# Kernel tuning notes

Hardware: AMD Instinct MI355X
Metric: run time of the kernel (lower is better)

## Reference

```python
import jax, jax.numpy as jnp
import numpy as np

H, HKV, D, W = 64, 8, 64, 128          # heads, kv heads, head_dim, sliding window
G = H // HKV                            # query heads per kv head
HID = 2880
THETA = 150000.0
SCALE = D ** -0.5
NEG = -1e30


def _rope(x, positions):
    # x: [B,S,h,D]; GPT-NeoX style rotate_half RoPE
    half = D // 2
    inv_freq = 1.0 / (THETA ** (jnp.arange(0, half, dtype=jnp.float32) / half))
    ang = positions.astype(jnp.float32)[:, None] * inv_freq          # [S, D/2]
    cos = jnp.cos(ang)[None, :, None, :]
    sin = jnp.sin(ang)[None, :, None, :]
    x1, x2 = x[..., :half], x[..., half:]
    return jnp.concatenate([x1 * cos - x2 * sin, x2 * cos + x1 * sin], axis=-1)


def setup_inputs() -> dict:
    key = jax.random.key(0)
    ks = jax.random.split(key, 6)
    B, S = 1, 2048
    return {
        "hidden_states": jax.random.normal(ks[0], (B, S, HID), jnp.float32),
        "positions": jnp.arange(S, dtype=jnp.int32),
        "w_qkv": jax.random.normal(ks[1], (HID, (H + 2 * HKV) * D), jnp.float32) * 0.02,
        "b_qkv": jax.random.normal(ks[2], ((H + 2 * HKV) * D,), jnp.float32) * 0.02,
        "w_o": jax.random.normal(ks[3], (H * D, HID), jnp.float32) * 0.02,
        "b_o": jax.random.normal(ks[4], (HID,), jnp.float32) * 0.02,
        "sinks": jax.random.normal(ks[5], (H,), jnp.float32),
    }


def reference(hidden_states, positions, w_qkv, b_qkv, w_o, b_o, sinks):
    B, S, _ = hidden_states.shape
    qkv = hidden_states @ w_qkv + b_qkv                               # [B,S,(H+2Hkv)*D]
    q, k, v = jnp.split(qkv, [H * D, H * D + HKV * D], axis=-1)
    Q = q.reshape(B, S, H, D)
    K = k.reshape(B, S, HKV, D)
    V = v.reshape(B, S, HKV, D)
    Q = _rope(Q, positions)
    K = _rope(K, positions)

    # banded (sliding-window) key/value gather: query i sees keys i-W+1..i
    offsets = jnp.arange(W) - (W - 1)                                 # [-(W-1)..0]
    kidx = jnp.arange(S)[:, None] + offsets                           # [S,W]
    valid = kidx >= 0
    kidx = jnp.maximum(kidx, 0)
    Kw = K[:, kidx]                                                    # [B,S,W,HKV,D]
    Vw = V[:, kidx]

    Qr = Q.reshape(B, S, HKV, G, D)                                    # GQA grouping
    scores = jnp.einsum('bskgd,bswkd->bskgw', Qr, Kw) * SCALE          # [B,S,HKV,G,W]
    scores = jnp.where(valid[None, :, None, None, :], scores, NEG)

    sink = sinks.reshape(HKV, G)[None, None]                           # [1,1,HKV,G]
    m = jnp.maximum(scores.max(axis=-1), sink)                         # [B,S,HKV,G]
    p = jnp.exp(scores - m[..., None])
    denom = p.sum(axis=-1) + jnp.exp(sink - m)                         # sink in normalizer
    out = jnp.einsum('bskgw,bswkd->bskgd', p, Vw) / denom[..., None]

    out = out.reshape(B, S, H * D)
    return out @ w_o + b_o
```

## Files before the change

### kernel.cpp

```cpp
#include <hip/hip_runtime.h>

typedef unsigned short u16;
typedef __bf16 bf16x8 __attribute__((ext_vector_type(8)));
typedef float f32x4 __attribute__((ext_vector_type(4)));
typedef unsigned short u16x8 __attribute__((ext_vector_type(8)));

#define QKV_N 5120
#define SEQ 2048
#define ATTN_K 4096
#define KPAD 2944
#define SCALE 0.125f
#define NEGINF -1e30f

__device__ __forceinline__ u16 f2bf(float f) {
  unsigned int u = __builtin_bit_cast(unsigned int, f);
  u = (u + 0x7FFFu + ((u >> 16) & 1u)) >> 16;
  return (u16)u;
}
__device__ __forceinline__ float bf2f(u16 u) {
  unsigned int x = ((unsigned int)u) << 16;
  return __builtin_bit_cast(float, x);
}

#define MFMA16(a, b, c) __builtin_amdgcn_mfma_f32_16x16x32_bf16((a), (b), (c), 0, 0, 0)

__device__ __forceinline__ void gl_lds16(const u16* g, u16* l) {
  __builtin_amdgcn_global_load_lds(
      (const __attribute__((address_space(1))) unsigned int*)(const void*)g,
      (__attribute__((address_space(3))) unsigned int*)(void*)l, 16, 0, 0);
}

__device__ __forceinline__ bf16x8 fragrd(const u16* base, int row, int rb) {
  return *(const bf16x8*)((const char*)(base + row * 32) + rb);
}

__device__ __forceinline__ bf16x8 lds_frag(const u16* mat, int row, int kh, int lg) {
  int off = row * 128 + ((kh * 64 + lg * 16) ^ ((row & 7) << 4));
  return *(const bf16x8*)((const char*)mat + off);
}

__global__ __launch_bounds__(256) void k_rope_table(const int* __restrict__ pos,
                                                    float2* __restrict__ tab) {
  int t = blockIdx.x * 256 + threadIdx.x;
  int s = t >> 5, i = t & 31;
  float freq = powf(150000.0f, -(float)i * (1.0f / 32.0f));
  float ang = (float)pos[s] * freq;
  float sv, cv;
  sincosf(ang, &sv, &cv);
  tab[t] = make_float2(cv, sv);
}

__global__ __launch_bounds__(256) void k_convert_pad(const float* __restrict__ in,
                                                     u16* __restrict__ out) {
  int i = blockIdx.x * 256 + threadIdx.x;
  int r = i / 736, c4 = i - r * 736;
  if (r >= 2048) return;
  ushort4 o = {0, 0, 0, 0};
  if (c4 < 720) {
    float4 v = *(const float4*)(in + (size_t)r * 2880 + c4 * 4);
    o.x = f2bf(v.x); o.y = f2bf(v.y); o.z = f2bf(v.z); o.w = f2bf(v.w);
  }
  ((ushort4*)out)[(size_t)r * 736 + c4] = o;
}

__global__ __launch_bounds__(256) void k_transpose(const float* __restrict__ in,
                                                   u16* __restrict__ out,
                                                   int Kin, int Kout, int Nd, int Npad) {
  __shared__ float tile[32][33];
  int n0 = blockIdx.x * 32, k0 = blockIdx.y * 32;
  int c = threadIdx.x & 31, r0 = threadIdx.x >> 5;
#pragma unroll
  for (int j = 0; j < 4; j++) {
    int r = r0 + j * 8;
    float v = 0.f;
    if (n0 + c < Nd && k0 + r < Kin) v = in[(size_t)(k0 + r) * Nd + n0 + c];
    tile[r][c] = v;
  }
  __syncthreads();
#pragma unroll
  for (int j = 0; j < 4; j++) {
    int rr = r0 + j * 8;
    int n = n0 + rr;
    if (n < Npad) out[(size_t)n * Kout + k0 + c] = f2bf(tile[c][rr]);
  }
}

__global__ __launch_bounds__(256, 2) void k_gemm1(const u16* __restrict__ Ag,
                                                  const u16* __restrict__ Bg,
                                                  const float* __restrict__ bias,
                                                  u16* __restrict__ C) {
  __shared__ u16 lds_[2][18432];
  u16* L = &lds_[0][0];
  const int tid = threadIdx.x;
  const int lane = tid & 63, wave = tid >> 6;
  const int wm = wave >> 1, wn = wave & 1;
  const int lr = lane & 15, lg = lane >> 4;
  const int bid = blockIdx.x;
  const int sb = (bid & 7) * 64 + (bid >> 3);
  const int m0 = (sb >> 5) * 128, n0 = (sb & 31) * 160;

  f32x4 acc[4][5] = {};
  bf16x8 Bf[5], Af0, Af1;

  const int rb = (lg * 16) ^ (((lr >> 1) & 3) << 4);
  const int arow = tid >> 2;
  const int axs = ((tid & 3) ^ ((tid >> 3) & 3)) << 3;

  size_t boff[5];
#pragma unroll
  for (int r_ = 0; r_ < 5; r_++) {
    int e = r_ * 2048 + tid * 8;
    int bkh = (e >= 5120) ? 1 : 0;
    int re = e - bkh * 5120;
    int brow = re >> 5;
    int bch = (re >> 3) & 3;
    int bps = bch ^ ((brow >> 1) & 3);
    boff[r_] = (size_t)(n0 + brow) * KPAD + bkh * 32 + bps * 8;
  }

#define STA(b, kh, kt, r_)                                                      \
  gl_lds16(Ag + (size_t)(m0 + (r_) * 64 + arow) * KPAD + (kt) + (kh) * 32 + axs, \
           L + (b) * 18432 + (kh) * 4096 + (r_) * 2048 + wave * 512)
#define STB(b, kt, r_)                                                          \
  gl_lds16(Bg + boff[r_] + (kt), L + (b) * 18432 + 8192 + (r_) * 2048 + wave * 512)
#define RDB(b, kh)                                                              \
  { _Pragma("unroll") for (int nf = 0; nf < 5; nf++)                            \
      Bf[nf] = fragrd(L + (b) * 18432 + 8192 + (kh) * 5120,                     \
                      wn * 80 + nf * 16 + lr, rb); }
#define RDA(b, kh, mf0_)                                                        \
  { Af0 = fragrd(L + (b) * 18432 + (kh) * 4096, wm * 64 + (mf0_) * 16 + lr, rb); \
    Af1 = fragrd(L + (b) * 18432 + (kh) * 4096, wm * 64 + ((mf0_) + 1) * 16 + lr, rb); }
#define MM(ma, mb)                                                              \
  { __builtin_amdgcn_s_setprio(1);                                              \
    _Pragma("unroll") for (int nf = 0; nf < 5; nf++) {                          \
      acc[ma][nf] = MFMA16(Af0, Bf[nf], acc[ma][nf]);                           \
      acc[mb][nf] = MFMA16(Af1, Bf[nf], acc[mb][nf]); }                         \
    __builtin_amdgcn_s_setprio(0); }
#define BAR __builtin_amdgcn_s_barrier();
#define VM4 asm volatile("s_waitcnt vmcnt(4)" ::: "memory");
#define VM0 asm volatile("s_waitcnt vmcnt(0)" ::: "memory");

  STA(0, 0, 0, 0); STA(0, 0, 0, 1);
  STB(0, 0, 0); STB(0, 0, 1); STB(0, 0, 2); STB(0, 0, 3); STB(0, 0, 4);
  STA(0, 1, 0, 0); STA(0, 1, 0, 1);
  VM4 BAR

  for (int t = 0; t < 46; t++) {
    const int b = t & 1, nb = b ^ 1;
    const int kt1 = (t + 1) * 64;
    const bool st = (t < 45);
    RDB(b, 0) RDA(b, 0, 0)
    if (st) { STA(nb, 0, kt1, 0); STA(nb, 0, kt1, 1); STB(nb, kt1, 0); }
    BAR MM(0, 1) BAR
    RDA(b, 0, 2)
    if (st) { STB(nb, kt1, 1); STB(nb, kt1, 2); VM4 } else { VM0 }
    BAR MM(2, 3) BAR
    RDB(b, 1) RDA(b, 1, 0)
    if (st) { STB(nb, kt1, 3); STB(nb, kt1, 4); }
    BAR MM(0, 1) BAR
    RDA(b, 1, 2)
    if (st) { STA(nb, 1, kt1, 0); STA(nb, 1, kt1, 1); VM4 }
    BAR MM(2, 3) BAR
  }
#undef STA
#undef STB
#undef RDB
#undef RDA
#undef MM
#undef BAR
#undef VM4
#undef VM0

#pragma unroll
  for (int mf = 0; mf < 4; mf++)
#pragma unroll
    for (int nf = 0; nf < 5; nf++) {
      int col = n0 + wn * 80 + nf * 16 + lr;
      float bv = bias[col];
#pragma unroll
      for (int rg = 0; rg < 4; rg++) {
        int row = m0 + wm * 64 + mf * 16 + lg * 4 + rg;
        C[(size_t)row * QKV_N + col] = f2bf(acc[mf][nf][rg] + bv);
      }
    }
}

__global__ __launch_bounds__(256, 2) void k_gemm2(const u16* __restrict__ Ag,
                                                  const u16* __restrict__ Bg,
                                                  const float* __restrict__ bias,
                                                  float* __restrict__ C) {
  __shared__ u16 ldsbuf[2][16384];
  const int tid = threadIdx.x;
  const int lane = tid & 63, wave = tid >> 6;
  const int wm = wave >> 1, wn = wave & 1;
  const int lr = lane & 15, lg = lane >> 4;
  int bid = blockIdx.x;
  int sb = (bid & 7) * 46 + (bid >> 3);
  const int m0 = (sb / 23) * 128, n0 = (sb % 23) * 128;

  f32x4 acc[4][4] = {};

  const int srow = wave * 8 + (lane >> 3);
  const int sc = ((lane & 7) ^ (lane >> 3)) << 3;
  const u16* gA = Ag + (size_t)(m0 + srow) * ATTN_K + sc;
  const u16* gB = Bg + (size_t)(n0 + srow) * ATTN_K + sc;

#define G2_STAGE(kt, b)                                                          \
  {                                                                              \
    u16* Ab = &ldsbuf[b][0];                                                     \
    u16* Bb = &ldsbuf[b][8192];                                                  \
    _Pragma("unroll") for (int r = 0; r < 4; r++) {                              \
      gl_lds16(gA + (size_t)(r * 32) * ATTN_K + (kt), Ab + (r * 32 + wave * 8) * 64); \
      gl_lds16(gB + (size_t)(r * 32) * ATTN_K + (kt), Bb + (r * 32 + wave * 8) * 64); \
    }                                                                            \
  }

  G2_STAGE(0, 0)
  G2_STAGE(64, 1)
  asm volatile("s_waitcnt vmcnt(8)" ::: "memory");
  __builtin_amdgcn_s_barrier();

  for (int t = 0; t < 64; t++) {
    const int b = t & 1;
    const u16* La = &ldsbuf[b][0];
    const u16* Lb = &ldsbuf[b][8192];
    bf16x8 Bf[4][2];
#pragma unroll
    for (int nf = 0; nf < 4; nf++)
#pragma unroll
      for (int kh = 0; kh < 2; kh++)
        Bf[nf][kh] = lds_frag(Lb, wn * 64 + nf * 16 + lr, kh, lg);
    bf16x8 Af[2][2];
#pragma unroll
    for (int mi = 0; mi < 2; mi++)
#pragma unroll
      for (int kh = 0; kh < 2; kh++)
        Af[mi][kh] = lds_frag(La, wm * 64 + mi * 16 + lr, kh, lg);
#pragma unroll
    for (int q = 0; q < 2; q++) {
      bf16x8 An[2][2];
      if (q < 1) {
#pragma unroll
        for (int mi = 0; mi < 2; mi++)
#pragma unroll
          for (int kh = 0; kh < 2; kh++)
            An[mi][kh] = lds_frag(La, wm * 64 + ((q + 1) * 2 + mi) * 16 + lr, kh, lg);
      }
      __builtin_amdgcn_s_setprio(1);
#pragma unroll
      for (int mi = 0; mi < 2; mi++)
#pragma unroll
        for (int nf = 0; nf < 4; nf++)
#pragma unroll
          for (int kh = 0; kh < 2; kh++)
            acc[q * 2 + mi][nf] = MFMA16(Af[mi][kh], Bf[nf][kh], acc[q * 2 + mi][nf]);
      __builtin_amdgcn_s_setprio(0);
      if (q < 1) {
#pragma unroll
        for (int mi = 0; mi < 2; mi++)
#pragma unroll
          for (int kh = 0; kh < 2; kh++)
            Af[mi][kh] = An[mi][kh];
      }
    }
    __builtin_amdgcn_s_barrier();
    if (t <= 61) {
      G2_STAGE((t + 2) * 64, b)
      asm volatile("s_waitcnt vmcnt(8)" ::: "memory");
    } else {
      asm volatile("s_waitcnt vmcnt(0)" ::: "memory");
    }
    __builtin_amdgcn_s_barrier();
  }
#undef G2_STAGE

#pragma unroll
  for (int mi = 0; mi < 4; mi++)
#pragma unroll
    for (int ni = 0; ni < 4; ni++) {
      int row = m0 + wm * 64 + mi * 16 + lg * 4;
      int col = n0 + wn * 64 + ni * 16 + lr;
      if (col < 2880) {
        float bv = bias[col];
#pragma unroll
        for (int rg = 0; rg < 4; rg++)
          C[(size_t)(row + rg) * 2880 + col] = acc[mi][ni][rg] + bv;
      }
    }
}

__global__ __launch_bounds__(512, 2) void k_attn(const u16* __restrict__ qkv,
                                                 const float* __restrict__ sinks,
                                                 const float2* __restrict__ tab,
                                                 u16* __restrict__ out) {
  __shared__ u16 Klds[160 * 64];
  __shared__ u16 Vt[64 * 168];
  __shared__ u16 Pslab[8 * 32 * 40];
  const int hk = blockIdx.y;
  const int s0 = blockIdx.x * 32;
  const int kb = s0 - 127;
  const int tid = threadIdx.x;
  const int lane = tid & 63, w = tid >> 6;
  const int lr = lane & 15, lg = lane >> 4;

  for (int u = tid; u < 160 * 4; u += 512) {
    int key = u >> 2, c = u & 3;
    int kidx = kb + key;
    u16x8 v1 = {0, 0, 0, 0, 0, 0, 0, 0}, v2 = v1;
    if (kidx >= 0 && kidx < SEQ) {
      const u16* base = qkv + (size_t)kidx * QKV_N + 4096 + hk * 64;
      u16x8 x1 = *(const u16x8*)(base + c * 8);
      u16x8 x2 = *(const u16x8*)(base + 32 + c * 8);
      const float2* cs = tab + (size_t)kidx * 32 + c * 8;
#pragma unroll
      for (int j = 0; j < 8; j++) {
        float f1 = bf2f(x1[j]), f2 = bf2f(x2[j]);
        float2 t = cs[j];
        v1[j] = f2bf(f1 * t.x - f2 * t.y);
        v2[j] = f2bf(f2 * t.x + f1 * t.y);
      }
    }
    int o1 = (key * 128 + c * 16) ^ ((key & 7) << 4);
    int o2 = (key * 128 + (c + 4) * 16) ^ ((key & 7) << 4);
    *(u16x8*)((char*)Klds + o1) = v1;
    *(u16x8*)((char*)Klds + o2) = v2;
  }
  for (int e4 = tid; e4 < 160 * 16; e4 += 512) {
    int key = e4 >> 4, d0 = (e4 & 15) * 4;
    int kidx = kb + key;
    ushort4 v = {0, 0, 0, 0};
    if (kidx >= 0 && kidx < SEQ)
      v = *(const ushort4*)(qkv + (size_t)kidx * QKV_N + 4608 + hk * 64 + d0);
    Vt[(d0 + 0) * 168 + key] = v.x;
    Vt[(d0 + 1) * 168 + key] = v.y;
    Vt[(d0 + 2) * 168 + key] = v.z;
    Vt[(d0 + 3) * 168 + key] = v.w;
  }

  const int head = hk * 8 + w;
  bf16x8 qf[2][2];
#pragma unroll
  for (int rt = 0; rt < 2; rt++) {
    int s = s0 + rt * 16 + lr;
    const u16* base = qkv + (size_t)s * QKV_N + head * 64 + lg * 8;
    u16x8 r0 = *(const u16x8*)(base);
    u16x8 r1 = *(const u16x8*)(base + 32);
    const float2* cs = tab + (size_t)s * 32 + lg * 8;
    u16x8 y0, y1;
#pragma unroll
    for (int j = 0; j < 8; j++) {
      float f1 = bf2f(r0[j]), f2 = bf2f(r1[j]);
      float2 t = cs[j];
      y0[j] = f2bf(f1 * t.x - f2 * t.y);
      y1[j] = f2bf(f2 * t.x + f1 * t.y);
    }
    qf[rt][0] = __builtin_bit_cast(bf16x8, y0);
    qf[rt][1] = __builtin_bit_cast(bf16x8, y1);
  }
  __syncthreads();

  f32x4 sc[2][10];
  f32x4 zz = {0.f, 0.f, 0.f, 0.f};
#pragma unroll
  for (int rt = 0; rt < 2; rt++)
#pragma unroll
    for (int nt = 0; nt < 10; nt++) sc[rt][nt] = zz;
#pragma unroll
  for (int nt = 0; nt < 10; nt++) {
    int key = nt * 16 + lr;
#pragma unroll
    for (int ks = 0; ks < 2; ks++) {
      int off = (key * 128 + ks * 64 + lg * 16) ^ ((key & 7) << 4);
      bf16x8 kf = *(const bf16x8*)((const char*)Klds + off);
      sc[0][nt] = MFMA16(qf[0][ks], kf, sc[0][nt]);
      sc[1][nt] = MFMA16(qf[1][ks], kf, sc[1][nt]);
    }
  }

#pragma unroll
  for (int rt = 0; rt < 2; rt++)
#pragma unroll
    for (int nt = 0; nt < 10; nt++)
#pragma unroll
      for (int rg = 0; rg < 4; rg++) {
        int qq = rt * 16 + lg * 4 + rg;
        int j = nt * 16 + lr;
        bool valid = (j >= qq) && (j <= qq + 127) && ((kb + j) >= 0);
        sc[rt][nt][rg] = valid ? sc[rt][nt][rg] * SCALE : NEGINF;
      }

  const float sink = sinks[head];
  float den[2][4];
#pragma unroll
  for (int rt = 0; rt < 2; rt++)
#pragma unroll
    for (int rg = 0; rg < 4; rg++) {
      float m = NEGINF;
#pragma unroll
      for (int nt = 0; nt < 10; nt++) m = fmaxf(m, sc[rt][nt][rg]);
#pragma unroll
      for (int x = 1; x < 16; x <<= 1) m = fmaxf(m, __shfl_xor(m, x, 64));
      m = fmaxf(m, sink);
      float sum = 0.f;
#pragma unroll
      for (int nt = 0; nt < 10; nt++) {
        float p = __expf(sc[rt][nt][rg] - m);
        sc[rt][nt][rg] = p;
        sum += p;
      }
#pragma unroll
      for (int x = 1; x < 16; x <<= 1) sum += __shfl_xor(sum, x, 64);
      den[rt][rg] = sum + __expf(sink - m);
    }

  f32x4 oacc[2][4];
#pragma unroll
  for (int rt = 0; rt < 2; rt++)
#pragma unroll
    for (int dn = 0; dn < 4; dn++) oacc[rt][dn] = zz;
  u16* slab = &Pslab[w * 32 * 40];
#pragma unroll
  for (int kt = 0; kt < 5; kt++) {
#pragma unroll
    for (int rt = 0; rt < 2; rt++)
#pragma unroll
      for (int j2 = 0; j2 < 2; j2++)
#pragma unroll
        for (int rg = 0; rg < 4; rg++)
          slab[(rt * 16 + lg * 4 + rg) * 40 + j2 * 16 + lr] = f2bf(sc[rt][kt * 2 + j2][rg]);
    asm volatile("s_waitcnt lgkmcnt(0)" ::: "memory");
    __builtin_amdgcn_sched_barrier(0);
    bf16x8 pf0 = *(const bf16x8*)&slab[lr * 40 + lg * 8];
    bf16x8 pf1 = *(const bf16x8*)&slab[(16 + lr) * 40 + lg * 8];
#pragma unroll
    for (int dn = 0; dn < 4; dn++) {
      bf16x8 vf = *(const bf16x8*)&Vt[(dn * 16 + lr) * 168 + kt * 32 + lg * 8];
      oacc[0][dn] = MFMA16(pf0, vf, oacc[0][dn]);
      oacc[1][dn] = MFMA16(pf1, vf, oacc[1][dn]);
    }
  }

#pragma unroll
  for (int rt = 0; rt < 2; rt++)
#pragma unroll
    for (int dn = 0; dn < 4; dn++)
#pragma unroll
      for (int rg = 0; rg < 4; rg++) {
        int s = s0 + rt * 16 + lg * 4 + rg;
        float val = oacc[rt][dn][rg] / den[rt][rg];
        out[(size_t)s * ATTN_K + head * 64 + dn * 16 + lr] = f2bf(val);
      }
}

extern "C" void kernel_launch(void* const* d_in, const int* in_sizes, int n_in,
                              void* d_out, int out_size, void* d_ws, size_t ws_size,
                              hipStream_t stream) {
  const float* hs = (const float*)d_in[0];
  const int* pos = (const int*)d_in[1];
  const float* wqkv = (const float*)d_in[2];
  const float* bqkv = (const float*)d_in[3];
  const float* wo = (const float*)d_in[4];
  const float* bo = (const float*)d_in[5];
  const float* sinks = (const float*)d_in[6];
  float* out = (float*)d_out;

  char* ws = (char*)d_ws;
  u16* qkvb = (u16*)(ws + 0);
  u16* hsb = (u16*)(ws + 41943040);
  u16* wqkvT = (u16*)(ws + 54001664);
  u16* attnb = (u16*)(ws + 41943040);
  u16* woT = (u16*)(ws + 84148224);
  float2* tab = (float2*)(ws + 108265472);

  k_rope_table<<<256, 256, 0, stream>>>(pos, tab);
  k_convert_pad<<<5888, 256, 0, stream>>>(hs, hsb);
  k_transpose<<<dim3(160, 92), 256, 0, stream>>>(wqkv, wqkvT, 2880, KPAD, 5120, 5120);
  k_transpose<<<dim3(92, 128), 256, 0, stream>>>(wo, woT, 4096, 4096, 2880, 2944);
  k_gemm1<<<512, 256, 0, stream>>>(hsb, wqkvT, bqkv, qkvb);
  k_attn<<<dim3(64, 8), 512, 0, stream>>>(qkvb, sinks, tab, attnb);
  k_gemm2<<<368, 256, 0, stream>>>(attnb, woT, bo, out);
}
```

Measured before the change: 202.3 us.

## Retile output GEMM to 128x96 tiles with gemm1-style interleaved load/MFMA pipeline

The output projection GEMM switches from 128x128 tiles (368 blocks) to 128x96 tiles (512 blocks), padding the transposed w_o to 3072 columns. The main loop is restructured to match gemm1's schedule: fine-grained global-to-LDS loads of the next stage are interleaved with four MFMA phases per k-tile, with partial vmcnt waits and an XOR-swizzled split-K LDS layout. The aim is better CU occupancy and wave balance, plus more overlap of memory with compute. In exchange it adds more barriers per iteration, reads A more often, and does extra padded work.

Result: slower. 209.7 us (+3.7%).

```diff
diff --git a/kernel.cpp b/kernel.cpp
--- a/kernel.cpp
+++ b/kernel.cpp
@@ -32,11 +32,6 @@
 
 __device__ __forceinline__ bf16x8 fragrd(const u16* base, int row, int rb) {
   return *(const bf16x8*)((const char*)(base + row * 32) + rb);
-}
-
-__device__ __forceinline__ bf16x8 lds_frag(const u16* mat, int row, int kh, int lg) {
-  int off = row * 128 + ((kh * 64 + lg * 16) ^ ((row & 7) << 4));
-  return *(const bf16x8*)((const char*)mat + off);
 }
 
 __global__ __launch_bounds__(256) void k_rope_table(const int* __restrict__ pos,
@@ -167,9 +162,6 @@
 #undef RDB
 #undef RDA
 #undef MM
-#undef BAR
-#undef VM4
-#undef VM0
 
 #pragma unroll
   for (int mf = 0; mf < 4; mf++)
@@ -189,102 +181,101 @@
                                                   const u16* __restrict__ Bg,
                                                   const float* __restrict__ bias,
                                                   float* __restrict__ C) {
-  __shared__ u16 ldsbuf[2][16384];
+  __shared__ u16 lds_[2][14336];
+  u16* L = &lds_[0][0];
   const int tid = threadIdx.x;
   const int lane = tid & 63, wave = tid >> 6;
   const int wm = wave >> 1, wn = wave & 1;
   const int lr = lane & 15, lg = lane >> 4;
-  int bid = blockIdx.x;
-  int sb = (bid & 7) * 46 + (bid >> 3);
-  const int m0 = (sb / 23) * 128, n0 = (sb % 23) * 128;
-
-  f32x4 acc[4][4] = {};
-
-  const int srow = wave * 8 + (lane >> 3);
-  const int sc = ((lane & 7) ^ (lane >> 3)) << 3;
-  const u16* gA = Ag + (size_t)(m0 + srow) * ATTN_K + sc;
-  const u16* gB = Bg + (size_t)(n0 + srow) * ATTN_K + sc;
-
-#define G2_STAGE(kt, b)                                                          \
-  {                                                                              \
-    u16* Ab = &ldsbuf[b][0];                                                     \
-    u16* Bb = &ldsbuf[b][8192];                                                  \
-    _Pragma("unroll") for (int r = 0; r < 4; r++) {                              \
-      gl_lds16(gA + (size_t)(r * 32) * ATTN_K + (kt), Ab + (r * 32 + wave * 8) * 64); \
-      gl_lds16(gB + (size_t)(r * 32) * ATTN_K + (kt), Bb + (r * 32 + wave * 8) * 64); \
-    }                                                                            \
-  }
-
-  G2_STAGE(0, 0)
-  G2_STAGE(64, 1)
-  asm volatile("s_waitcnt vmcnt(8)" ::: "memory");
-  __builtin_amdgcn_s_barrier();
+  const int bid = blockIdx.x;
+  const int sb = (bid & 7) * 64 + (bid >> 3);
+  const int m0 = (sb >> 5) * 128, n0 = (sb & 31) * 96;
+
+  f32x4 acc[4][3] = {};
+  bf16x8 Bf[3], Af0, Af1;
+
+  const int rb = (lg * 16) ^ (((lr >> 1) & 3) << 4);
+  const int arow = tid >> 2;
+  const int axs = ((tid & 3) ^ ((tid >> 3) & 3)) << 3;
+
+  size_t boff[3];
+#pragma unroll
+  for (int r_ = 0; r_ < 3; r_++) {
+    int e = r_ * 2048 + tid * 8;
+    int bkh = (e >= 3072) ? 1 : 0;
+    int re = e - bkh * 3072;
+    int brow = re >> 5;
+    int bch = (re >> 3) & 3;
+    int bps = bch ^ ((brow >> 1) & 3);
+    boff[r_] = (size_t)(n0 + brow) * ATTN_K + bkh * 32 + bps * 8;
+  }
+
+#define STA2(b, kh, kt, r_)                                                     \
+  gl_lds16(Ag + (size_t)(m0 + (r_) * 64 + arow) * ATTN_K + (kt) + (kh) * 32 + axs, \
+           L + (b) * 14336 + (kh) * 4096 + (r_) * 2048 + wave * 512)
+#define STB2(b, kt, r_)                                                         \
+  gl_lds16(Bg + boff[r_] + (kt), L + (b) * 14336 + 8192 + (r_) * 2048 + wave * 512)
+#define RDB2(b, kh)                                                             \
+  { _Pragma("unroll") for (int nf = 0; nf < 3; nf++)                            \
+      Bf[nf] = fragrd(L + (b) * 14336 + 8192 + (kh) * 3072,                     \
+                      wn * 48 + nf * 16 + lr, rb); }
+#define RDA2(b, kh, mf0_)                                                       \
+  { Af0 = fragrd(L + (b) * 14336 + (kh) * 4096, wm * 64 + (mf0_) * 16 + lr, rb); \
+    Af1 = fragrd(L + (b) * 14336 + (kh) * 4096, wm * 64 + ((mf0_) + 1) * 16 + lr, rb); }
+#define MM2(ma, mb)                                                             \
+  { __builtin_amdgcn_s_setprio(1);                                              \
+    _Pragma("unroll") for (int nf = 0; nf < 3; nf++) {                          \
+      acc[ma][nf] = MFMA16(Af0, Bf[nf], acc[ma][nf]);                           \
+      acc[mb][nf] = MFMA16(Af1, Bf[nf], acc[mb][nf]); }                         \
+    __builtin_amdgcn_s_setprio(0); }
+#define VM5 asm volatile("s_waitcnt vmcnt(5)" ::: "memory");
+#define VM2 asm volatile("s_waitcnt vmcnt(2)" ::: "memory");
+
+  STA2(0, 0, 0, 0); STA2(0, 0, 0, 1);
+  STB2(0, 0, 0); STB2(0, 0, 1); STB2(0, 0, 2);
+  STA2(0, 1, 0, 0); STA2(0, 1, 0, 1);
+  VM2 BAR
 
   for (int t = 0; t < 64; t++) {
-    const int b = t & 1;
-    const u16* La = &ldsbuf[b][0];
-    const u16* Lb = &ldsbuf[b][8192];
-    bf16x8 Bf[4][2];
-#pragma unroll
-    for (int nf = 0; nf < 4; nf++)
-#pragma unroll
-      for (int kh = 0; kh < 2; kh++)
-        Bf[nf][kh] = lds_frag(Lb, wn * 64 + nf * 16 + lr, kh, lg);
-    bf16x8 Af[2][2];
-#pragma unroll
-    for (int mi = 0; mi < 2; mi++)
-#pragma unroll
-      for (int kh = 0; kh < 2; kh++)
-        Af[mi][kh] = lds_frag(La, wm * 64 + mi * 16 + lr, kh, lg);
-#pragma unroll
-    for (int q = 0; q < 2; q++) {
-      bf16x8 An[2][2];
-      if (q < 1) {
-#pragma unroll
-        for (int mi = 0; mi < 2; mi++)
-#pragma unroll
-          for (int kh = 0; kh < 2; kh++)
-            An[mi][kh] = lds_frag(La, wm * 64 + ((q + 1) * 2 + mi) * 16 + lr, kh, lg);
-      }
-      __builtin_amdgcn_s_setprio(1);
-#pragma unroll
-      for (int mi = 0; mi < 2; mi++)
-#pragma unroll
-        for (int nf = 0; nf < 4; nf++)
-#pragma unroll
-          for (int kh = 0; kh < 2; kh++)
-            acc[q * 2 + mi][nf] = MFMA16(Af[mi][kh], Bf[nf][kh], acc[q * 2 + mi][nf]);
-      __builtin_amdgcn_s_setprio(0);
-      if (q < 1) {
-#pragma unroll
-        for (int mi = 0; mi < 2; mi++)
-#pragma unroll
-          for (int kh = 0; kh < 2; kh++)
-            Af[mi][kh] = An[mi][kh];
-      }
-    }
-    __builtin_amdgcn_s_barrier();
-    if (t <= 61) {
-      G2_STAGE((t + 2) * 64, b)
-      asm volatile("s_waitcnt vmcnt(8)" ::: "memory");
-    } else {
-      asm volatile("s_waitcnt vmcnt(0)" ::: "memory");
-    }
-    __builtin_amdgcn_s_barrier();
-  }
-#undef G2_STAGE
-
-#pragma unroll
-  for (int mi = 0; mi < 4; mi++)
-#pragma unroll
-    for (int ni = 0; ni < 4; ni++) {
-      int row = m0 + wm * 64 + mi * 16 + lg * 4;
-      int col = n0 + wn * 64 + ni * 16 + lr;
+    const int b = t & 1, nb = b ^ 1;
+    const int kt1 = (t + 1) * 64;
+    const bool st = (t < 63);
+    RDB2(b, 0) RDA2(b, 0, 0)
+    if (st) { STA2(nb, 0, kt1, 0); STA2(nb, 0, kt1, 1); STB2(nb, kt1, 0); }
+    BAR MM2(0, 1) BAR
+    RDA2(b, 0, 2)
+    if (st) { STB2(nb, kt1, 1); STB2(nb, kt1, 2); VM5 } else { VM0 }
+    BAR MM2(2, 3) BAR
+    RDB2(b, 1) RDA2(b, 1, 0)
+    if (st) { STA2(nb, 1, kt1, 0); }
+    BAR MM2(0, 1) BAR
+    RDA2(b, 1, 2)
+    if (st) { STA2(nb, 1, kt1, 1); VM2 }
+    BAR MM2(2, 3) BAR
+  }
+#undef STA2
+#undef STB2
+#undef RDB2
+#undef RDA2
+#undef MM2
+#undef VM5
+#undef VM2
+#undef BAR
+#undef VM4
+#undef VM0
+
+#pragma unroll
+  for (int mf = 0; mf < 4; mf++)
+#pragma unroll
+    for (int nf = 0; nf < 3; nf++) {
+      int col = n0 + wn * 48 + nf * 16 + lr;
       if (col < 2880) {
         float bv = bias[col];
 #pragma unroll
-        for (int rg = 0; rg < 4; rg++)
-          C[(size_t)(row + rg) * 2880 + col] = acc[mi][ni][rg] + bv;
+        for (int rg = 0; rg < 4; rg++) {
+          int row = m0 + wm * 64 + mf * 16 + lg * 4 + rg;
+          C[(size_t)row * 2880 + col] = acc[mf][nf][rg] + bv;
+        }
       }
     }
 }
@@ -470,13 +461,13 @@
   u16* wqkvT = (u16*)(ws + 54001664);
   u16* attnb = (u16*)(ws + 41943040);
   u16* woT = (u16*)(ws + 84148224);
-  float2* tab = (float2*)(ws + 108265472);
+  float2* tab = (float2*)(ws + 109314048);
 
   k_rope_table<<<256, 256, 0, stream>>>(pos, tab);
   k_convert_pad<<<5888, 256, 0, stream>>>(hs, hsb);
   k_transpose<<<dim3(160, 92), 256, 0, stream>>>(wqkv, wqkvT, 2880, KPAD, 5120, 5120);
-  k_transpose<<<dim3(92, 128), 256, 0, stream>>>(wo, woT, 4096, 4096, 2880, 2944);
+  k_transpose<<<dim3(96, 128), 256, 0, stream>>>(wo, woT, 4096, 4096, 2880, 3072);
   k_gemm1<<<512, 256, 0, stream>>>(hsb, wqkvT, bqkv, qkvb);
   k_attn<<<dim3(64, 8), 512, 0, stream>>>(qkvb, sinks, tab, attnb);
-  k_gemm2<<<368, 256, 0, stream>>>(attnb, woT, bo, out);
-}
+  k_gemm2<<<512, 256, 0, stream>>>(attnb, woT, bo, out);
+}
```
